# Kernel optimization log

Hardware: AMD Instinct MI355X
Metric: run time of the kernel (lower is better)

The kernel has to match this reference:

```python
import jax, jax.numpy as jnp
import numpy as np

N = 8192
IN_FEATURES = 768
OUT_FEATURES = 128


def setup_inputs() -> dict:
    key = jax.random.key(0)
    k_h, k_adj, k_w, k_a = jax.random.split(key, 4)
    H = jax.random.normal(k_h, (N, IN_FEATURES), dtype=jnp.float32)
    adj = (jax.random.uniform(k_adj, (N, N)) > 0.5).astype(jnp.float32)
    # xavier_uniform with gain=1.414
    gain = 1.414
    limit_w = gain * np.sqrt(6.0 / (IN_FEATURES + OUT_FEATURES))
    W = jax.random.uniform(k_w, (IN_FEATURES, OUT_FEATURES), dtype=jnp.float32,
                           minval=-limit_w, maxval=limit_w)
    limit_a = gain * np.sqrt(6.0 / (2 * OUT_FEATURES + 1))
    a = jax.random.uniform(k_a, (2 * OUT_FEATURES, 1), dtype=jnp.float32,
                           minval=-limit_a, maxval=limit_a)
    return {"H": H, "adj": adj, "W": W, "a": a}


def reference(H, adj, W, a):
    # H: [N, F_in], adj: [N, N], W: [F_in, F_out], a: [2*F_out, 1]
    Hp = H @ W  # [N, F_out]
    # concat([h_i, h_j]) @ a  ==  h_i @ a[:F] + h_j @ a[F:]
    F_out = Hp.shape[1]
    src = Hp @ a[:F_out]   # [N, 1]
    dst = Hp @ a[F_out:]   # [N, 1]
    scores = src + dst.T   # [N, N]
    # Faithful to original: masked entries stay 0 (not -inf),
    # leaky_relu then full-row softmax including the zeros.
    att = jnp.where(adj != 0, scores, jnp.zeros((), dtype=scores.dtype))
    att = jax.nn.leaky_relu(att, negative_slope=0.2)
    att = jax.nn.softmax(att, axis=1)
    return att @ Hp  # [N, F_out]
```

## Files before the change

kernel.cpp:

```cpp
#include <hip/hip_runtime.h>
#include <hip/hip_bf16.h>
#include <stdint.h>

#define N_NODES 8192
#define F_IN    768
#define F_OUT   128

typedef _Float16 f16_t;
typedef _Float16 f16x8 __attribute__((ext_vector_type(8)));
typedef _Float16 f16x4 __attribute__((ext_vector_type(4)));
typedef float  f32x4  __attribute__((ext_vector_type(4)));
typedef unsigned short u16x4 __attribute__((ext_vector_type(4)));

static __device__ __forceinline__ unsigned short f16_bits(float x) {
  f16_t h = (f16_t)x;
  return __builtin_bit_cast(unsigned short, h);
}

static __device__ __forceinline__ void gload_lds16(const void* g, void* l) {
  __builtin_amdgcn_global_load_lds(
      (const __attribute__((address_space(1))) unsigned int*)g,
      (__attribute__((address_space(3))) unsigned int*)l, 16, 0, 0);
}

__global__ __launch_bounds__(256) void prep_wt(const float* __restrict__ W,
                                               f16_t* __restrict__ WT) {
  int gid = blockIdx.x * 256 + threadIdx.x;
  int col = gid / 192;
  int kq  = gid % 192;
  int k0  = kq * 4;
  u16x4 u;
#pragma unroll
  for (int i = 0; i < 4; ++i)
    u[i] = f16_bits(W[(k0 + i) * F_OUT + col]);
  *(u16x4*)(WT + col * F_IN + k0) = u;
}

__global__ __launch_bounds__(256) void prep_waux(const float* __restrict__ W,
                                                 const float* __restrict__ a,
                                                 float* __restrict__ wxs,
                                                 float* __restrict__ wxd) {
  const int wave = threadIdx.x >> 6;
  const int lane = threadIdx.x & 63;
  const int row  = blockIdx.x * 4 + wave;
  float w0 = W[row * F_OUT + lane];
  float w1 = W[row * F_OUT + 64 + lane];
  float s = w0 * a[lane]       + w1 * a[64 + lane];
  float d = w0 * a[128 + lane] + w1 * a[192 + lane];
#pragma unroll
  for (int m = 1; m <= 32; m <<= 1) {
    s += __shfl_xor(s, m);
    d += __shfl_xor(d, m);
  }
  if (lane == 0) { wxs[row] = s; wxd[row] = d; }
}

__global__ __launch_bounds__(256, 2) void hp_kernel(
    const float* __restrict__ H, const f16_t* __restrict__ WT,
    const float* __restrict__ wxs, const float* __restrict__ wxd,
    f16_t* __restrict__ HpP, float* __restrict__ srcv, float* __restrict__ dstv)
{
  __shared__ unsigned short h_s[32 * 64];
  __shared__ float ws_s[F_IN];
  __shared__ float wd_s[F_IN];

  const int tid  = threadIdx.x;
  const int wave = tid >> 6;
  const int lane = tid & 63;
  const int l15  = lane & 15;
  const int g    = lane >> 4;
  const int row0 = blockIdx.x * 32;
  const int lrow = tid >> 4;
  const int q    = tid & 15;

  for (int i = tid; i < F_IN; i += 256) { ws_s[i] = wxs[i]; wd_s[i] = wxd[i]; }

  f32x4 zero4 = {0.f, 0.f, 0.f, 0.f};
  f32x4 acc[2][2];
#pragma unroll
  for (int i = 0; i < 2; ++i)
#pragma unroll
    for (int j = 0; j < 2; ++j) acc[i][j] = zero4;
  float ps0 = 0.f, ps1 = 0.f, pd0 = 0.f, pd1 = 0.f;

  __syncthreads();

  for (int c = 0; c < F_IN / 64; ++c) {
    const int k0 = c * 64;
    f32x4 h0 = *(const f32x4*)&H[(size_t)(row0 + lrow) * F_IN + k0 + q * 4];
    f32x4 h1 = *(const f32x4*)&H[(size_t)(row0 + 16 + lrow) * F_IN + k0 + q * 4];
    f32x4 as = *(const f32x4*)&ws_s[k0 + q * 4];
    f32x4 ad = *(const f32x4*)&wd_s[k0 + q * 4];
#pragma unroll
    for (int e = 0; e < 4; ++e) {
      ps0 += h0[e] * as[e]; pd0 += h0[e] * ad[e];
      ps1 += h1[e] * as[e]; pd1 += h1[e] * ad[e];
    }
    u16x4 u0, u1;
#pragma unroll
    for (int e = 0; e < 4; ++e) { u0[e] = f16_bits(h0[e]); u1[e] = f16_bits(h1[e]); }
    const int g8 = q >> 1, hh = (q & 1) * 4;
    *(u16x4*)&h_s[lrow * 64 + ((g8 ^ (lrow & 7)) * 8) + hh] = u0;
    const int r1 = lrow + 16;
    *(u16x4*)&h_s[r1 * 64 + ((g8 ^ (r1 & 7)) * 8) + hh] = u1;
    __syncthreads();

#pragma unroll
    for (int mt = 0; mt < 2; ++mt) {
      const int arow = mt * 16 + l15;
#pragma unroll
      for (int s = 0; s < 2; ++s) {
        f16x8 af = *(const f16x8*)&h_s[arow * 64 + (((s * 4 + g) ^ (arow & 7)) * 8)];
#pragma unroll
        for (int ntl = 0; ntl < 2; ++ntl) {
          const int nt = wave * 2 + ntl;
          f16x8 bfv = *(const f16x8*)&WT[(size_t)(nt * 16 + l15) * F_IN + k0 + s * 32 + g * 8];
          acc[mt][ntl] = __builtin_amdgcn_mfma_f32_16x16x32_f16(af, bfv, acc[mt][ntl], 0, 0, 0);
        }
      }
    }
    __syncthreads();
  }

#pragma unroll
  for (int m = 1; m <= 8; m <<= 1) {
    ps0 += __shfl_xor(ps0, m); ps1 += __shfl_xor(ps1, m);
    pd0 += __shfl_xor(pd0, m); pd1 += __shfl_xor(pd1, m);
  }
  if (q == 0) {
    srcv[row0 + lrow] = ps0; srcv[row0 + 16 + lrow] = ps1;
    dstv[row0 + lrow] = pd0; dstv[row0 + 16 + lrow] = pd1;
  }

  const int j32 = row0 >> 5;
#pragma unroll
  for (int mt = 0; mt < 2; ++mt)
#pragma unroll
    for (int ntl = 0; ntl < 2; ++ntl) {
      const int ntB = wave * 2 + ntl;
      const int gB  = mt * 2 + (g >> 1);
      f16x4 v;
#pragma unroll
      for (int r = 0; r < 4; ++r) v[r] = (f16_t)acc[mt][ntl][r];
      const size_t elem = ((size_t)(j32 * 8 + ntB)) * 512 + (gB * 16 + l15) * 8 + (g & 1) * 4;
      *(f16x4*)(HpP + elem) = v;
    }
}

__global__ __launch_bounds__(512, 4) void attn_kernel(
    const float* __restrict__ adj, const f16_t* __restrict__ HpP,
    const float* __restrict__ srcv, const float* __restrict__ dstv,
    float* __restrict__ out)
{
  __shared__ __align__(16) float dst_s[N_NODES];
  __shared__ __align__(16) float adj_s[2][4096];
  __shared__ float zred[8][16];
  __shared__ float mred[8];

  const int tid  = threadIdx.x;
  const int wave = tid >> 6;
  const int lane = tid & 63;
  const int l15  = lane & 15;
  const int g    = lane >> 4;
  const int row0 = blockIdx.x * 16;

#define STAGE(buf, tt)                                                         \
  do {                                                                         \
    _Pragma("unroll")                                                          \
    for (int rr = 0; rr < 2; ++rr) {                                           \
      const int r = wave * 2 + rr;                                             \
      const float* gp = adj + (size_t)(row0 + r) * N_NODES + (tt) * 256 +      \
                        ((lane ^ (r & 7)) << 2);                               \
      gload_lds16(gp, &adj_s[buf][r * 256]);                                   \
    }                                                                          \
  } while (0)

  STAGE(0, 0);

  float mloc = -3.0e38f;
  for (int i = tid; i < N_NODES / 4; i += 512) {
    f32x4 v = ((const f32x4*)dstv)[i];
    ((f32x4*)dst_s)[i] = v;
    mloc = fmaxf(mloc, fmaxf(fmaxf(v[0], v[1]), fmaxf(v[2], v[3])));
  }
#pragma unroll
  for (int m = 1; m <= 32; m <<= 1) mloc = fmaxf(mloc, __shfl_xor(mloc, m));
  if (lane == 0) mred[wave] = mloc;

  const float my_src = srcv[row0 + l15];
  __syncthreads();

  float maxdst = mred[0];
#pragma unroll
  for (int w2 = 1; w2 < 8; ++w2) maxdst = fmaxf(maxdst, mred[w2]);
  const float Mi    = fmaxf(0.f, my_src + maxdst);
  const float wmask = __expf(-Mi);

  const int swz  = l15 & 7;
  const int uA   = wave * 8 + g * 2;
  const int offA = l15 * 256 + ((uA ^ swz) << 2);
  const int offB = l15 * 256 + (((uA + 1) ^ swz) << 2);
  const int dstoff = wave * 32 + g * 8;

  f32x4 zero4 = {0.f, 0.f, 0.f, 0.f};
  f32x4 acc[8];
#pragma unroll
  for (int nt = 0; nt < 8; ++nt) acc[nt] = zero4;
  float z_acc = 0.f;

  for (int t = 0; t < 32; ++t) {
    const int cur = t & 1;
    if (t < 31) STAGE(cur ^ 1, t + 1);

    const f16_t* hb = HpP + ((size_t)(t * 8 + wave) * 8) * 512 + lane * 8;
    f16x8 bf[8];
#pragma unroll
    for (int nt = 0; nt < 8; ++nt) bf[nt] = *(const f16x8*)(hb + nt * 512);

    const float* ab = &adj_s[cur][0];
    f32x4 a0 = *(const f32x4*)(ab + offA);
    f32x4 a1 = *(const f32x4*)(ab + offB);
    f32x4 d0 = *(const f32x4*)&dst_s[t * 256 + dstoff];
    f32x4 d1 = *(const f32x4*)&dst_s[t * 256 + dstoff + 4];

    f16x8 afr;
#pragma unroll
    for (int e = 0; e < 4; ++e) {
      float s  = my_src + d0[e];
      float lr = fmaxf(s, 0.2f * s);
      float w  = (a0[e] != 0.f) ? __expf(lr - Mi) : wmask;
      f16_t wq = (f16_t)w;
      z_acc += (float)wq;
      afr[e] = wq;
    }
#pragma unroll
    for (int e = 0; e < 4; ++e) {
      float s  = my_src + d1[e];
      float lr = fmaxf(s, 0.2f * s);
      float w  = (a1[e] != 0.f) ? __expf(lr - Mi) : wmask;
      f16_t wq = (f16_t)w;
      z_acc += (float)wq;
      afr[4 + e] = wq;
    }

#pragma unroll
    for (int nt = 0; nt < 8; ++nt)
      acc[nt] = __builtin_amdgcn_mfma_f32_16x16x32_f16(afr, bf[nt], acc[nt], 0, 0, 0);

    __syncthreads();
  }

  float zc = z_acc + __shfl_xor(z_acc, 16);
  zc += __shfl_xor(zc, 32);
  if (lane < 16) zred[wave][lane] = zc;
  __syncthreads();

  float* part = &adj_s[0][0];
  if (wave < 4) {
#pragma unroll
    for (int nt = 0; nt < 8; ++nt)
#pragma unroll
      for (int r = 0; r < 4; ++r)
        part[wave * 2048 + (g * 4 + r) * 128 + nt * 16 + l15] = acc[nt][r];
  }
  __syncthreads();
  if (wave >= 4) {
#pragma unroll
    for (int nt = 0; nt < 8; ++nt)
#pragma unroll
      for (int r = 0; r < 4; ++r)
        part[(wave - 4) * 2048 + (g * 4 + r) * 128 + nt * 16 + l15] += acc[nt][r];
  }
  __syncthreads();
  {
    const int orow = tid >> 5;
    const int c0   = (tid & 31) * 4;
    f32x4 s = zero4;
#pragma unroll
    for (int b = 0; b < 4; ++b)
      s += *(const f32x4*)&part[b * 2048 + orow * 128 + c0];
    float zt = 0.f;
#pragma unroll
    for (int w2 = 0; w2 < 8; ++w2) zt += zred[w2][orow];
    *(f32x4*)&out[(size_t)(row0 + orow) * F_OUT + c0] = s * (1.0f / zt);
  }
#undef STAGE
}

extern "C" void kernel_launch(void* const* d_in, const int* in_sizes, int n_in,
                              void* d_out, int out_size, void* d_ws, size_t ws_size,
                              hipStream_t stream) {
  const float* H   = (const float*)d_in[0];
  const float* adj = (const float*)d_in[1];
  const float* W   = (const float*)d_in[2];
  const float* a   = (const float*)d_in[3];
  float* out = (float*)d_out;

  char* ws = (char*)d_ws;
  f16_t* HpP  = (f16_t*)(ws);
  f16_t* WT   = (f16_t*)(ws + 2097152);
  float* wxs  = (float*)(ws + 2293760);
  float* wxd  = (float*)(ws + 2296832);
  float* srcv = (float*)(ws + 2299904);
  float* dstv = (float*)(ws + 2332672);

  prep_wt   <<<dim3(96),  dim3(256), 0, stream>>>(W, WT);
  prep_waux <<<dim3(192), dim3(256), 0, stream>>>(W, a, wxs, wxd);
  hp_kernel <<<dim3(256), dim3(256), 0, stream>>>(H, WT, wxs, wxd, HpP, srcv, dstv);
  attn_kernel<<<dim3(512), dim3(512), 0, stream>>>(adj, HpP, srcv, dstv, out);
}
```

Baseline: 410.5 us.

## Merge prep kernels, halve hp tile, pipeline attn adjacency loads with explicit waitcnt

Merges the two weight-prep kernels into one launch. Halves the row tile in hp_kernel so it launches twice as many blocks. In attn_kernel, drops the 32KB dst_s LDS copy and reads dst values from global memory instead, which shrinks LDS use and raises launch_bounds occupancy to 8. The adjacency staging becomes a two-deep prefetch using explicit vmcnt waits and raw barriers. The risk is extra global/L2 traffic for dst reads and fragile hand-placed waitcnt ordering, since the HpP loads also count against vmcnt.

```diff
diff --git a/kernel.cpp b/kernel.cpp
--- a/kernel.cpp
+++ b/kernel.cpp
@@ -23,36 +23,36 @@
       (__attribute__((address_space(3))) unsigned int*)l, 16, 0, 0);
 }
 
-__global__ __launch_bounds__(256) void prep_wt(const float* __restrict__ W,
-                                               f16_t* __restrict__ WT) {
-  int gid = blockIdx.x * 256 + threadIdx.x;
-  int col = gid / 192;
-  int kq  = gid % 192;
-  int k0  = kq * 4;
-  u16x4 u;
-#pragma unroll
-  for (int i = 0; i < 4; ++i)
-    u[i] = f16_bits(W[(k0 + i) * F_OUT + col]);
-  *(u16x4*)(WT + col * F_IN + k0) = u;
-}
-
-__global__ __launch_bounds__(256) void prep_waux(const float* __restrict__ W,
-                                                 const float* __restrict__ a,
-                                                 float* __restrict__ wxs,
-                                                 float* __restrict__ wxd) {
-  const int wave = threadIdx.x >> 6;
-  const int lane = threadIdx.x & 63;
-  const int row  = blockIdx.x * 4 + wave;
-  float w0 = W[row * F_OUT + lane];
-  float w1 = W[row * F_OUT + 64 + lane];
-  float s = w0 * a[lane]       + w1 * a[64 + lane];
-  float d = w0 * a[128 + lane] + w1 * a[192 + lane];
-#pragma unroll
-  for (int m = 1; m <= 32; m <<= 1) {
-    s += __shfl_xor(s, m);
-    d += __shfl_xor(d, m);
-  }
-  if (lane == 0) { wxs[row] = s; wxd[row] = d; }
+__global__ __launch_bounds__(256) void prep(const float* __restrict__ W,
+                                            const float* __restrict__ a,
+                                            f16_t* __restrict__ WT,
+                                            float* __restrict__ wxs,
+                                            float* __restrict__ wxd) {
+  if (blockIdx.x < 96) {
+    int gid = blockIdx.x * 256 + threadIdx.x;
+    int col = gid / 192;
+    int kq  = gid % 192;
+    int k0  = kq * 4;
+    u16x4 u;
+#pragma unroll
+    for (int i = 0; i < 4; ++i)
+      u[i] = f16_bits(W[(k0 + i) * F_OUT + col]);
+    *(u16x4*)(WT + col * F_IN + k0) = u;
+  } else {
+    const int wave = threadIdx.x >> 6;
+    const int lane = threadIdx.x & 63;
+    const int row  = (blockIdx.x - 96) * 4 + wave;
+    float w0 = W[row * F_OUT + lane];
+    float w1 = W[row * F_OUT + 64 + lane];
+    float s = w0 * a[lane]       + w1 * a[64 + lane];
+    float d = w0 * a[128 + lane] + w1 * a[192 + lane];
+#pragma unroll
+    for (int m = 1; m <= 32; m <<= 1) {
+      s += __shfl_xor(s, m);
+      d += __shfl_xor(d, m);
+    }
+    if (lane == 0) { wxs[row] = s; wxd[row] = d; }
+  }
 }
 
 __global__ __launch_bounds__(256, 2) void hp_kernel(
@@ -60,7 +60,7 @@
     const float* __restrict__ wxs, const float* __restrict__ wxd,
     f16_t* __restrict__ HpP, float* __restrict__ srcv, float* __restrict__ dstv)
 {
-  __shared__ unsigned short h_s[32 * 64];
+  __shared__ unsigned short h_s[16 * 64];
   __shared__ float ws_s[F_IN];
   __shared__ float wd_s[F_IN];
 
@@ -69,54 +69,43 @@
   const int lane = tid & 63;
   const int l15  = lane & 15;
   const int g    = lane >> 4;
-  const int row0 = blockIdx.x * 32;
+  const int row0 = blockIdx.x * 16;
   const int lrow = tid >> 4;
   const int q    = tid & 15;
 
   for (int i = tid; i < F_IN; i += 256) { ws_s[i] = wxs[i]; wd_s[i] = wxd[i]; }
 
   f32x4 zero4 = {0.f, 0.f, 0.f, 0.f};
-  f32x4 acc[2][2];
-#pragma unroll
-  for (int i = 0; i < 2; ++i)
-#pragma unroll
-    for (int j = 0; j < 2; ++j) acc[i][j] = zero4;
-  float ps0 = 0.f, ps1 = 0.f, pd0 = 0.f, pd1 = 0.f;
+  f32x4 acc[2];
+  acc[0] = zero4; acc[1] = zero4;
+  float ps0 = 0.f, pd0 = 0.f;
 
   __syncthreads();
 
   for (int c = 0; c < F_IN / 64; ++c) {
     const int k0 = c * 64;
     f32x4 h0 = *(const f32x4*)&H[(size_t)(row0 + lrow) * F_IN + k0 + q * 4];
-    f32x4 h1 = *(const f32x4*)&H[(size_t)(row0 + 16 + lrow) * F_IN + k0 + q * 4];
     f32x4 as = *(const f32x4*)&ws_s[k0 + q * 4];
     f32x4 ad = *(const f32x4*)&wd_s[k0 + q * 4];
 #pragma unroll
     for (int e = 0; e < 4; ++e) {
       ps0 += h0[e] * as[e]; pd0 += h0[e] * ad[e];
-      ps1 += h1[e] * as[e]; pd1 += h1[e] * ad[e];
-    }
-    u16x4 u0, u1;
-#pragma unroll
-    for (int e = 0; e < 4; ++e) { u0[e] = f16_bits(h0[e]); u1[e] = f16_bits(h1[e]); }
+    }
+    u16x4 u0;
+#pragma unroll
+    for (int e = 0; e < 4; ++e) u0[e] = f16_bits(h0[e]);
     const int g8 = q >> 1, hh = (q & 1) * 4;
     *(u16x4*)&h_s[lrow * 64 + ((g8 ^ (lrow & 7)) * 8) + hh] = u0;
-    const int r1 = lrow + 16;
-    *(u16x4*)&h_s[r1 * 64 + ((g8 ^ (r1 & 7)) * 8) + hh] = u1;
     __syncthreads();
 
 #pragma unroll
-    for (int mt = 0; mt < 2; ++mt) {
-      const int arow = mt * 16 + l15;
-#pragma unroll
-      for (int s = 0; s < 2; ++s) {
-        f16x8 af = *(const f16x8*)&h_s[arow * 64 + (((s * 4 + g) ^ (arow & 7)) * 8)];
-#pragma unroll
-        for (int ntl = 0; ntl < 2; ++ntl) {
-          const int nt = wave * 2 + ntl;
-          f16x8 bfv = *(const f16x8*)&WT[(size_t)(nt * 16 + l15) * F_IN + k0 + s * 32 + g * 8];
-          acc[mt][ntl] = __builtin_amdgcn_mfma_f32_16x16x32_f16(af, bfv, acc[mt][ntl], 0, 0, 0);
-        }
+    for (int s = 0; s < 2; ++s) {
+      f16x8 af = *(const f16x8*)&h_s[l15 * 64 + (((s * 4 + g) ^ (l15 & 7)) * 8)];
+#pragma unroll
+      for (int ntl = 0; ntl < 2; ++ntl) {
+        const int nt = wave * 2 + ntl;
+        f16x8 bfv = *(const f16x8*)&WT[(size_t)(nt * 16 + l15) * F_IN + k0 + s * 32 + g * 8];
+        acc[ntl] = __builtin_amdgcn_mfma_f32_16x16x32_f16(af, bfv, acc[ntl], 0, 0, 0);
       }
     }
     __syncthreads();
@@ -124,35 +113,30 @@
 
 #pragma unroll
   for (int m = 1; m <= 8; m <<= 1) {
-    ps0 += __shfl_xor(ps0, m); ps1 += __shfl_xor(ps1, m);
-    pd0 += __shfl_xor(pd0, m); pd1 += __shfl_xor(pd1, m);
-  }
-  if (q == 0) {
-    srcv[row0 + lrow] = ps0; srcv[row0 + 16 + lrow] = ps1;
-    dstv[row0 + lrow] = pd0; dstv[row0 + 16 + lrow] = pd1;
-  }
-
-  const int j32 = row0 >> 5;
-#pragma unroll
-  for (int mt = 0; mt < 2; ++mt)
-#pragma unroll
-    for (int ntl = 0; ntl < 2; ++ntl) {
-      const int ntB = wave * 2 + ntl;
-      const int gB  = mt * 2 + (g >> 1);
-      f16x4 v;
-#pragma unroll
-      for (int r = 0; r < 4; ++r) v[r] = (f16_t)acc[mt][ntl][r];
-      const size_t elem = ((size_t)(j32 * 8 + ntB)) * 512 + (gB * 16 + l15) * 8 + (g & 1) * 4;
-      *(f16x4*)(HpP + elem) = v;
-    }
-}
-
-__global__ __launch_bounds__(512, 4) void attn_kernel(
+    ps0 += __shfl_xor(ps0, m);
+    pd0 += __shfl_xor(pd0, m);
+  }
+  if (q == 0) { srcv[row0 + lrow] = ps0; dstv[row0 + lrow] = pd0; }
+
+  const int j32 = blockIdx.x >> 1;
+  const int mt  = blockIdx.x & 1;
+#pragma unroll
+  for (int ntl = 0; ntl < 2; ++ntl) {
+    const int ntB = wave * 2 + ntl;
+    const int gB  = mt * 2 + (g >> 1);
+    f16x4 v;
+#pragma unroll
+    for (int r = 0; r < 4; ++r) v[r] = (f16_t)acc[ntl][r];
+    const size_t elem = ((size_t)(j32 * 8 + ntB)) * 512 + (gB * 16 + l15) * 8 + (g & 1) * 4;
+    *(f16x4*)(HpP + elem) = v;
+  }
+}
+
+__global__ __launch_bounds__(512, 8) void attn_kernel(
     const float* __restrict__ adj, const f16_t* __restrict__ HpP,
     const float* __restrict__ srcv, const float* __restrict__ dstv,
     float* __restrict__ out)
 {
-  __shared__ __align__(16) float dst_s[N_NODES];
   __shared__ __align__(16) float adj_s[2][4096];
   __shared__ float zred[8][16];
   __shared__ float mred[8];
@@ -176,11 +160,11 @@
   } while (0)
 
   STAGE(0, 0);
+  STAGE(1, 1);
 
   float mloc = -3.0e38f;
   for (int i = tid; i < N_NODES / 4; i += 512) {
     f32x4 v = ((const f32x4*)dstv)[i];
-    ((f32x4*)dst_s)[i] = v;
     mloc = fmaxf(mloc, fmaxf(fmaxf(v[0], v[1]), fmaxf(v[2], v[3])));
   }
 #pragma unroll
@@ -210,7 +194,10 @@
 
   for (int t = 0; t < 32; ++t) {
     const int cur = t & 1;
-    if (t < 31) STAGE(cur ^ 1, t + 1);
+    if (t < 31) { asm volatile("s_waitcnt vmcnt(2)" ::: "memory"); }
+    else        { asm volatile("s_waitcnt vmcnt(0)" ::: "memory"); }
+    __builtin_amdgcn_s_barrier();
+    __builtin_amdgcn_sched_barrier(0);
 
     const f16_t* hb = HpP + ((size_t)(t * 8 + wave) * 8) * 512 + lane * 8;
     f16x8 bf[8];
@@ -220,8 +207,8 @@
     const float* ab = &adj_s[cur][0];
     f32x4 a0 = *(const f32x4*)(ab + offA);
     f32x4 a1 = *(const f32x4*)(ab + offB);
-    f32x4 d0 = *(const f32x4*)&dst_s[t * 256 + dstoff];
-    f32x4 d1 = *(const f32x4*)&dst_s[t * 256 + dstoff + 4];
+    f32x4 d0 = *(const f32x4*)&dstv[t * 256 + dstoff];
+    f32x4 d1 = *(const f32x4*)&dstv[t * 256 + dstoff + 4];
 
     f16x8 afr;
 #pragma unroll
@@ -247,7 +234,10 @@
     for (int nt = 0; nt < 8; ++nt)
       acc[nt] = __builtin_amdgcn_mfma_f32_16x16x32_f16(afr, bf[nt], acc[nt], 0, 0, 0);
 
-    __syncthreads();
+    __builtin_amdgcn_sched_barrier(0);
+    __builtin_amdgcn_s_barrier();
+    __builtin_amdgcn_sched_barrier(0);
+    if (t < 30) STAGE(cur, t + 2);
   }
 
   float zc = z_acc + __shfl_xor(z_acc, 16);
@@ -304,8 +294,7 @@
   float* srcv = (float*)(ws + 2299904);
   float* dstv = (float*)(ws + 2332672);
 
-  prep_wt   <<<dim3(96),  dim3(256), 0, stream>>>(W, WT);
-  prep_waux <<<dim3(192), dim3(256), 0, stream>>>(W, a, wxs, wxd);
-  hp_kernel <<<dim3(256), dim3(256), 0, stream>>>(H, WT, wxs, wxd, HpP, srcv, dstv);
+  prep      <<<dim3(288), dim3(256), 0, stream>>>(W, a, WT, wxs, wxd);
+  hp_kernel <<<dim3(512), dim3(256), 0, stream>>>(H, WT, wxs, wxd, HpP, srcv, dstv);
   attn_kernel<<<dim3(512), dim3(512), 0, stream>>>(adj, HpP, srcv, dstv, out);
 }
```

After: 488.2 us. +18.9%, slower.

## Restructure attention kernel to 32-row tiles with register-prefetched adjacency and fused prep

Applied to the files above, without the earlier changes.

The attention kernel now handles 32 rows per 1024-thread block. Adjacency is streamed through registers with nontemporal loads two tiles ahead, instead of through async global-to-LDS staging. The f16 attention weights are shared via LDS, and the K dimension is split across two wave halves, which cuts HpP re-reads per output row. The two prep kernels are merged into one launch, hp_kernel prefetches the next H chunk into registers, and plain barriers become explicit waitcnt plus sched barriers. The cost is fewer blocks (256 at occupancy 1) and higher register pressure, which may hurt latency hiding on the bandwidth-bound adj stream.

```diff
diff --git a/kernel.cpp b/kernel.cpp
--- a/kernel.cpp
+++ b/kernel.cpp
@@ -17,42 +17,43 @@
   return __builtin_bit_cast(unsigned short, h);
 }
 
-static __device__ __forceinline__ void gload_lds16(const void* g, void* l) {
-  __builtin_amdgcn_global_load_lds(
-      (const __attribute__((address_space(1))) unsigned int*)g,
-      (__attribute__((address_space(3))) unsigned int*)l, 16, 0, 0);
-}
-
-__global__ __launch_bounds__(256) void prep_wt(const float* __restrict__ W,
-                                               f16_t* __restrict__ WT) {
-  int gid = blockIdx.x * 256 + threadIdx.x;
-  int col = gid / 192;
-  int kq  = gid % 192;
-  int k0  = kq * 4;
-  u16x4 u;
-#pragma unroll
-  for (int i = 0; i < 4; ++i)
-    u[i] = f16_bits(W[(k0 + i) * F_OUT + col]);
-  *(u16x4*)(WT + col * F_IN + k0) = u;
-}
-
-__global__ __launch_bounds__(256) void prep_waux(const float* __restrict__ W,
-                                                 const float* __restrict__ a,
-                                                 float* __restrict__ wxs,
-                                                 float* __restrict__ wxd) {
-  const int wave = threadIdx.x >> 6;
-  const int lane = threadIdx.x & 63;
-  const int row  = blockIdx.x * 4 + wave;
-  float w0 = W[row * F_OUT + lane];
-  float w1 = W[row * F_OUT + 64 + lane];
-  float s = w0 * a[lane]       + w1 * a[64 + lane];
-  float d = w0 * a[128 + lane] + w1 * a[192 + lane];
-#pragma unroll
-  for (int m = 1; m <= 32; m <<= 1) {
-    s += __shfl_xor(s, m);
-    d += __shfl_xor(d, m);
-  }
-  if (lane == 0) { wxs[row] = s; wxd[row] = d; }
+static __device__ __forceinline__ void hard_barrier() {
+  asm volatile("s_waitcnt lgkmcnt(0)" ::: "memory");
+  __builtin_amdgcn_sched_barrier(0);
+  __builtin_amdgcn_s_barrier();
+  __builtin_amdgcn_sched_barrier(0);
+}
+
+__global__ __launch_bounds__(256) void prep(const float* __restrict__ W,
+                                            const float* __restrict__ a,
+                                            f16_t* __restrict__ WT,
+                                            float* __restrict__ wxs,
+                                            float* __restrict__ wxd) {
+  if (blockIdx.x < 96) {
+    int gid = blockIdx.x * 256 + threadIdx.x;
+    int col = gid / 192;
+    int kq  = gid % 192;
+    int k0  = kq * 4;
+    u16x4 u;
+#pragma unroll
+    for (int i = 0; i < 4; ++i)
+      u[i] = f16_bits(W[(k0 + i) * F_OUT + col]);
+    *(u16x4*)(WT + col * F_IN + k0) = u;
+  } else {
+    const int wave = threadIdx.x >> 6;
+    const int lane = threadIdx.x & 63;
+    const int row  = (blockIdx.x - 96) * 4 + wave;
+    float w0 = W[row * F_OUT + lane];
+    float w1 = W[row * F_OUT + 64 + lane];
+    float s = w0 * a[lane]       + w1 * a[64 + lane];
+    float d = w0 * a[128 + lane] + w1 * a[192 + lane];
+#pragma unroll
+    for (int m = 1; m <= 32; m <<= 1) {
+      s += __shfl_xor(s, m);
+      d += __shfl_xor(d, m);
+    }
+    if (lane == 0) { wxs[row] = s; wxd[row] = d; }
+  }
 }
 
 __global__ __launch_bounds__(256, 2) void hp_kernel(
@@ -85,10 +86,15 @@
 
   __syncthreads();
 
+  f32x4 h0 = *(const f32x4*)&H[(size_t)(row0 + lrow) * F_IN + q * 4];
+  f32x4 h1 = *(const f32x4*)&H[(size_t)(row0 + 16 + lrow) * F_IN + q * 4];
+
   for (int c = 0; c < F_IN / 64; ++c) {
     const int k0 = c * 64;
-    f32x4 h0 = *(const f32x4*)&H[(size_t)(row0 + lrow) * F_IN + k0 + q * 4];
-    f32x4 h1 = *(const f32x4*)&H[(size_t)(row0 + 16 + lrow) * F_IN + k0 + q * 4];
+    const int kn = (c < 11 ? c + 1 : 11) * 64;
+    f32x4 h0n = *(const f32x4*)&H[(size_t)(row0 + lrow) * F_IN + kn + q * 4];
+    f32x4 h1n = *(const f32x4*)&H[(size_t)(row0 + 16 + lrow) * F_IN + kn + q * 4];
+
     f32x4 as = *(const f32x4*)&ws_s[k0 + q * 4];
     f32x4 ad = *(const f32x4*)&wd_s[k0 + q * 4];
 #pragma unroll
@@ -103,7 +109,7 @@
     *(u16x4*)&h_s[lrow * 64 + ((g8 ^ (lrow & 7)) * 8) + hh] = u0;
     const int r1 = lrow + 16;
     *(u16x4*)&h_s[r1 * 64 + ((g8 ^ (r1 & 7)) * 8) + hh] = u1;
-    __syncthreads();
+    hard_barrier();
 
 #pragma unroll
     for (int mt = 0; mt < 2; ++mt) {
@@ -119,7 +125,8 @@
         }
       }
     }
-    __syncthreads();
+    hard_barrier();
+    h0 = h0n; h1 = h1n;
   }
 
 #pragma unroll
@@ -147,144 +154,132 @@
     }
 }
 
-__global__ __launch_bounds__(512, 4) void attn_kernel(
+__global__ __launch_bounds__(1024, 1) void attn_kernel(
     const float* __restrict__ adj, const f16_t* __restrict__ HpP,
     const float* __restrict__ srcv, const float* __restrict__ dstv,
     float* __restrict__ out)
 {
-  __shared__ __align__(16) float dst_s[N_NODES];
-  __shared__ __align__(16) float adj_s[2][4096];
-  __shared__ float zred[8][16];
-  __shared__ float mred[8];
-
-  const int tid  = threadIdx.x;
-  const int wave = tid >> 6;
-  const int lane = tid & 63;
-  const int l15  = lane & 15;
-  const int g    = lane >> 4;
-  const int row0 = blockIdx.x * 16;
-
-#define STAGE(buf, tt)                                                         \
-  do {                                                                         \
-    _Pragma("unroll")                                                          \
-    for (int rr = 0; rr < 2; ++rr) {                                           \
-      const int r = wave * 2 + rr;                                             \
-      const float* gp = adj + (size_t)(row0 + r) * N_NODES + (tt) * 256 +      \
-                        ((lane ^ (r & 7)) << 2);                               \
-      gload_lds16(gp, &adj_s[buf][r * 256]);                                   \
-    }                                                                          \
-  } while (0)
-
-  STAGE(0, 0);
+  __shared__ __align__(16) float smem[8192];
+  __shared__ float zred[32];
+  __shared__ float mred[16];
+
+  const int tid = threadIdx.x;
+  const int wv  = tid >> 6;
+  const int ln  = tid & 63;
+  const int l15 = ln & 15;
+  const int lg  = ln >> 4;
+  const int row0 = blockIdx.x * 32;
+
+  const int wr = tid >> 5;
+  const int wc = (tid & 31) * 8;
+  const int nt = wv & 7;
+  const int kh = wv >> 3;
+
+  unsigned short* w_s = (unsigned short*)smem;
+  const int gstore = wr * 32 + ((wc >> 3) ^ (wr & 7));
 
   float mloc = -3.0e38f;
-  for (int i = tid; i < N_NODES / 4; i += 512) {
-    f32x4 v = ((const f32x4*)dstv)[i];
-    ((f32x4*)dst_s)[i] = v;
+#pragma unroll
+  for (int i = 0; i < 2; ++i) {
+    f32x4 v = ((const f32x4*)dstv)[i * 1024 + tid];
     mloc = fmaxf(mloc, fmaxf(fmaxf(v[0], v[1]), fmaxf(v[2], v[3])));
   }
 #pragma unroll
   for (int m = 1; m <= 32; m <<= 1) mloc = fmaxf(mloc, __shfl_xor(mloc, m));
-  if (lane == 0) mred[wave] = mloc;
-
-  const float my_src = srcv[row0 + l15];
+  if (ln == 0) mred[wv] = mloc;
+  const float my_src = srcv[row0 + wr];
   __syncthreads();
-
   float maxdst = mred[0];
 #pragma unroll
-  for (int w2 = 1; w2 < 8; ++w2) maxdst = fmaxf(maxdst, mred[w2]);
-  const float Mi    = fmaxf(0.f, my_src + maxdst);
-  const float wmask = __expf(-Mi);
-
-  const int swz  = l15 & 7;
-  const int uA   = wave * 8 + g * 2;
-  const int offA = l15 * 256 + ((uA ^ swz) << 2);
-  const int offB = l15 * 256 + (((uA + 1) ^ swz) << 2);
-  const int dstoff = wave * 32 + g * 8;
+  for (int i = 1; i < 16; ++i) maxdst = fmaxf(maxdst, mred[i]);
+  const float Mi = fmaxf(0.f, my_src + maxdst);
+  const float wm = __expf(-Mi);
+
+  const float* adjr = adj + (size_t)(row0 + wr) * N_NODES + wc;
 
   f32x4 zero4 = {0.f, 0.f, 0.f, 0.f};
-  f32x4 acc[8];
-#pragma unroll
-  for (int nt = 0; nt < 8; ++nt) acc[nt] = zero4;
-  float z_acc = 0.f;
-
-  for (int t = 0; t < 32; ++t) {
-    const int cur = t & 1;
-    if (t < 31) STAGE(cur ^ 1, t + 1);
-
-    const f16_t* hb = HpP + ((size_t)(t * 8 + wave) * 8) * 512 + lane * 8;
-    f16x8 bf[8];
-#pragma unroll
-    for (int nt = 0; nt < 8; ++nt) bf[nt] = *(const f16x8*)(hb + nt * 512);
-
-    const float* ab = &adj_s[cur][0];
-    f32x4 a0 = *(const f32x4*)(ab + offA);
-    f32x4 a1 = *(const f32x4*)(ab + offB);
-    f32x4 d0 = *(const f32x4*)&dst_s[t * 256 + dstoff];
-    f32x4 d1 = *(const f32x4*)&dst_s[t * 256 + dstoff + 4];
-
-    f16x8 afr;
+  f32x4 acc0 = zero4, acc1 = zero4;
+  float z = 0.f;
+
+  f32x4 c0  = __builtin_nontemporal_load((const f32x4*)(adjr));
+  f32x4 c1  = __builtin_nontemporal_load((const f32x4*)(adjr + 4));
+  f32x4 cd0 = *(const f32x4*)(dstv + wc);
+  f32x4 cd1 = *(const f32x4*)(dstv + wc + 4);
+  f32x4 n0  = __builtin_nontemporal_load((const f32x4*)(adjr + 256));
+  f32x4 n1  = __builtin_nontemporal_load((const f32x4*)(adjr + 260));
+  f32x4 nd0 = *(const f32x4*)(dstv + 256 + wc);
+  f32x4 nd1 = *(const f32x4*)(dstv + 256 + wc + 4);
+
+  for (int s = 0; s < 32; ++s) {
+    const f16_t* hb = HpP + (((size_t)s * 8 + kh * 4) * 8 + nt) * 512 + ln * 8;
+    f16x8 bf0 = *(const f16x8*)(hb);
+    f16x8 bf1 = *(const f16x8*)(hb + 4096);
+    f16x8 bf2 = *(const f16x8*)(hb + 8192);
+    f16x8 bf3 = *(const f16x8*)(hb + 12288);
+
+    f16x8 wq;
 #pragma unroll
     for (int e = 0; e < 4; ++e) {
-      float s  = my_src + d0[e];
-      float lr = fmaxf(s, 0.2f * s);
-      float w  = (a0[e] != 0.f) ? __expf(lr - Mi) : wmask;
-      f16_t wq = (f16_t)w;
-      z_acc += (float)wq;
-      afr[e] = wq;
+      float sc = my_src + cd0[e];
+      float lr = fmaxf(sc, 0.2f * sc);
+      float w  = (c0[e] != 0.f) ? __expf(lr - Mi) : wm;
+      f16_t qv = (f16_t)w;
+      z += (float)qv;
+      wq[e] = qv;
     }
 #pragma unroll
     for (int e = 0; e < 4; ++e) {
-      float s  = my_src + d1[e];
-      float lr = fmaxf(s, 0.2f * s);
-      float w  = (a1[e] != 0.f) ? __expf(lr - Mi) : wmask;
-      f16_t wq = (f16_t)w;
-      z_acc += (float)wq;
-      afr[4 + e] = wq;
-    }
-
-#pragma unroll
-    for (int nt = 0; nt < 8; ++nt)
-      acc[nt] = __builtin_amdgcn_mfma_f32_16x16x32_f16(afr, bf[nt], acc[nt], 0, 0, 0);
-
-    __syncthreads();
-  }
-
-  float zc = z_acc + __shfl_xor(z_acc, 16);
-  zc += __shfl_xor(zc, 32);
-  if (lane < 16) zred[wave][lane] = zc;
-  __syncthreads();
-
-  float* part = &adj_s[0][0];
-  if (wave < 4) {
-#pragma unroll
-    for (int nt = 0; nt < 8; ++nt)
-#pragma unroll
-      for (int r = 0; r < 4; ++r)
-        part[wave * 2048 + (g * 4 + r) * 128 + nt * 16 + l15] = acc[nt][r];
-  }
-  __syncthreads();
-  if (wave >= 4) {
-#pragma unroll
-    for (int nt = 0; nt < 8; ++nt)
-#pragma unroll
-      for (int r = 0; r < 4; ++r)
-        part[(wave - 4) * 2048 + (g * 4 + r) * 128 + nt * 16 + l15] += acc[nt][r];
+      float sc = my_src + cd1[e];
+      float lr = fmaxf(sc, 0.2f * sc);
+      float w  = (c1[e] != 0.f) ? __expf(lr - Mi) : wm;
+      f16_t qv = (f16_t)w;
+      z += (float)qv;
+      wq[4 + e] = qv;
+    }
+
+    const int sp = (s < 30) ? s + 2 : 31;
+    f32x4 m0  = __builtin_nontemporal_load((const f32x4*)(adjr + sp * 256));
+    f32x4 m1  = __builtin_nontemporal_load((const f32x4*)(adjr + sp * 256 + 4));
+    f32x4 md0 = *(const f32x4*)(dstv + sp * 256 + wc);
+    f32x4 md1 = *(const f32x4*)(dstv + sp * 256 + wc + 4);
+
+    *(f16x8*)&w_s[gstore * 8] = wq;
+    hard_barrier();
+
+#pragma unroll
+    for (int k4 = 0; k4 < 4; ++k4) {
+      const int kk = kh * 4 + k4;
+      const int R0 = l15, R1 = 16 + l15;
+      f16x8 a0 = *(const f16x8*)&w_s[(R0 * 32 + ((kk * 4 + lg) ^ (R0 & 7))) * 8];
+      f16x8 a1 = *(const f16x8*)&w_s[(R1 * 32 + ((kk * 4 + lg) ^ (R1 & 7))) * 8];
+      f16x8 bb = (k4 == 0) ? bf0 : (k4 == 1) ? bf1 : (k4 == 2) ? bf2 : bf3;
+      acc0 = __builtin_amdgcn_mfma_f32_16x16x32_f16(a0, bb, acc0, 0, 0, 0);
+      acc1 = __builtin_amdgcn_mfma_f32_16x16x32_f16(a1, bb, acc1, 0, 0, 0);
+    }
+    hard_barrier();
+
+    c0 = n0; c1 = n1; cd0 = nd0; cd1 = nd1;
+    n0 = m0; n1 = m1; nd0 = md0; nd1 = md1;
+  }
+
+#pragma unroll
+  for (int m = 1; m <= 16; m <<= 1) z += __shfl_xor(z, m);
+  if ((tid & 31) == 0) zred[wr] = z;
+
+#pragma unroll
+  for (int r = 0; r < 4; ++r) {
+    smem[kh * 4096 + (lg * 4 + r) * 128 + nt * 16 + l15]        = acc0[r];
+    smem[kh * 4096 + (16 + lg * 4 + r) * 128 + nt * 16 + l15]   = acc1[r];
   }
   __syncthreads();
   {
     const int orow = tid >> 5;
-    const int c0   = (tid & 31) * 4;
-    f32x4 s = zero4;
-#pragma unroll
-    for (int b = 0; b < 4; ++b)
-      s += *(const f32x4*)&part[b * 2048 + orow * 128 + c0];
-    float zt = 0.f;
-#pragma unroll
-    for (int w2 = 0; w2 < 8; ++w2) zt += zred[w2][orow];
-    *(f32x4*)&out[(size_t)(row0 + orow) * F_OUT + c0] = s * (1.0f / zt);
-  }
-#undef STAGE
+    const int c0o  = (tid & 31) * 4;
+    f32x4 p0 = *(const f32x4*)&smem[orow * 128 + c0o];
+    f32x4 p1 = *(const f32x4*)&smem[4096 + orow * 128 + c0o];
+    f32x4 res = (p0 + p1) * (1.0f / zred[orow]);
+    *(f32x4*)&out[(size_t)(row0 + orow) * F_OUT + c0o] = res;
+  }
 }
 
 extern "C" void kernel_launch(void* const* d_in, const int* in_sizes, int n_in,
@@ -304,8 +299,7 @@
   float* srcv = (float*)(ws + 2299904);
   float* dstv = (float*)(ws + 2332672);
 
-  prep_wt   <<<dim3(96),  dim3(256), 0, stream>>>(W, WT);
-  prep_waux <<<dim3(192), dim3(256), 0, stream>>>(W, a, wxs, wxd);
+  prep      <<<dim3(288), dim3(256), 0, stream>>>(W, a, WT, wxs, wxd);
   hp_kernel <<<dim3(256), dim3(256), 0, stream>>>(H, WT, wxs, wxd, HpP, srcv, dstv);
-  attn_kernel<<<dim3(512), dim3(512), 0, stream>>>(adj, HpP, srcv, dstv, out);
-}
+  attn_kernel<<<dim3(256), dim3(1024), 0, stream>>>(adj, HpP, srcv, dstv, out);
+}
```

New measurement: 401.2 us. 2.3% less time.
